# Performance work log

Hardware: AMD Instinct MI355X
Metric: run time of the kernel (lower is better)

## Reference

```python
import jax, jax.numpy as jnp
import numpy as np

N_HEADS = 4
SIGMA = 6.0
T_IN = 12
T_TOTAL = 24


def setup_inputs() -> dict:
    key = jax.random.key(0)
    k1, k2, k3, k4, k5 = jax.random.split(key, 5)
    B, T, N, C, K = 16, T_IN, 5000, 4, 16
    x = jax.random.normal(k1, (B, T, N, C), dtype=jnp.float32)
    dists = jax.random.uniform(k2, (N, K), dtype=jnp.float32) * 10.0  # kNN distances
    neighbors = jax.random.randint(k3, (N, K), 0, N)                  # kNN indices
    d_in = T * N_HEADS                   # 48
    d_out = T_TOTAL - T_IN               # 12
    W = jax.random.normal(k4, (d_in, d_out), dtype=jnp.float32) * (1.0 / np.sqrt(d_in))
    b = jax.random.normal(k5, (d_out,), dtype=jnp.float32) * 0.01
    return {"x": x, "dists": dists, "W": W, "b": b, "neighbors": neighbors}


def reference(x, dists, W, b, neighbors):
    B, T, N, C = x.shape
    H = N_HEADS
    # lambda_h = h/H for h = 1..H
    lam = jnp.arange(1, H + 1, dtype=x.dtype) / H                     # [H]
    # weights[n,k,h] = exp(-d_{nk}^2 * lam_h / sigma^2)
    w = jnp.exp(-(dists ** 2)[:, :, None] * lam / (SIGMA ** 2))       # [N,K,H]
    # gather neighbor features: [B,T,N,K,C]
    xg = x[:, :, neighbors, :]
    # distance-weighted aggregation over neighbors -> [B,T,N,H,C]
    agg = jnp.einsum('btnkc,nkh->btnhc', xg, w)
    # permute (0,2,4,1,3) -> [B,N,C,T,H], flatten last two -> [B,N,C,T*H]
    feat = jnp.transpose(agg, (0, 2, 4, 1, 3)).reshape(B, N, C, T * H)
    # shrink: Linear + ReLU -> [B,N,C,T_TOTAL-T]
    y = jax.nn.relu(feat @ W + b)
    # -> [B, T_TOTAL-T, N, C]
    y = jnp.transpose(y, (0, 3, 1, 2))
    return jnp.concatenate([x, y], axis=1)                            # [B,T_TOTAL,N,C]
```

## Files before the change

### kernel.cpp

```cpp
#include <hip/hip_runtime.h>

#define Bz 16
#define Tin 12
#define Ttot 24
#define NN 5000
#define Cc 4
#define KK 16
#define HH 4
#define OO 12
#define TH 48
#define BT 192
#define G  8
#define JJ 24

typedef float nfloat4 __attribute__((ext_vector_type(4)));

__device__ __forceinline__ float4 nt_load4(const float4* p) {
    nfloat4 v = __builtin_nontemporal_load((const nfloat4*)p);
    return *(float4*)&v;
}
__device__ __forceinline__ void nt_store4(float4 v, float4* p) {
    __builtin_nontemporal_store(*(nfloat4*)&v, (nfloat4*)p);
}

#define K1_NB 64
#define K1_BT 24

__global__ __launch_bounds__(256) void transpose_concat_kernel(
    const float4* __restrict__ x4,
    float4* __restrict__ xT2,
    float4* __restrict__ out4)
{
    __shared__ float4 tile[K1_BT][K1_NB + 1];
    const int n0  = blockIdx.x * K1_NB;
    const int g   = blockIdx.y;
    const int bt0 = g * K1_BT;
    const int rem = min(K1_NB, NN - n0);
    const int tid = threadIdx.x;

    #pragma unroll
    for (int r = 0; r < (K1_NB * K1_BT) / 256; r++) {
        int tau = r * 256 + tid;
        int j = tau / K1_NB;
        int i = tau % K1_NB;
        if (i < rem) {
            int bt = bt0 + j;
            float4 v = nt_load4(&x4[(size_t)bt * NN + n0 + i]);
            tile[j][i] = v;
            int b = bt / Tin, t = bt - b * Tin;
            nt_store4(v, &out4[(size_t)(b * Ttot + t) * NN + n0 + i]);
        }
    }
    __syncthreads();

    #pragma unroll
    for (int r = 0; r < (K1_NB * K1_BT) / 256; r++) {
        int tau = r * 256 + tid;
        int i = tau / K1_BT;
        int j = tau - i * K1_BT;
        if (i < rem) {
            xT2[((size_t)g * NN + (n0 + i)) * JJ + j] = tile[j][i];
        }
    }
}

#define NPB 8
#define FST 5
#define FSB 61
#define FSN 123

__global__ __launch_bounds__(192) void gnn_main_kernel(
    const float4* __restrict__ xT2,
    const float* __restrict__ dists,
    const float* __restrict__ W,
    const float* __restrict__ bias,
    const int*   __restrict__ nbrs,
    float4* __restrict__ out4)
{
    __shared__ float4 feat[NPB * FSN];
    __shared__ float4 w4_s[NPB][KK];
    __shared__ float  W_s[TH * OO];
    __shared__ float  bias_s[OO];
    __shared__ int    nbroff_s[NPB][KK];

    const int bid = blockIdx.x;
    const int g   = bid & 7;
    const int n0  = (bid >> 3) * NPB;
    const int tid = threadIdx.x;

    for (int i = tid; i < TH * OO; i += 192) W_s[i] = W[i];
    if (tid < OO) bias_s[tid] = bias[tid];
    if (tid < NPB * KK) {
        int nl = tid >> 4, k = tid & 15;
        nbroff_s[nl][k] = nbrs[(n0 + nl) * KK + k] * (JJ * (int)sizeof(float4));
        float d = dists[(n0 + nl) * KK + k];
        float p = expf(-(d * d) * (1.0f / 144.0f));
        float4 wv;
        wv.x = p;
        wv.y = p * p;
        wv.z = wv.y * p;
        wv.w = wv.y * wv.y;
        w4_s[nl][k] = wv;
    }
    __syncthreads();

    {
        const int nl  = tid / JJ;
        const int j   = tid - nl * JJ;
        const int b_l = j / Tin;
        const int t   = j - b_l * Tin;
        const char* xgb = (const char*)xT2 + (size_t)g * (NN * JJ * sizeof(float4));
        const unsigned j16 = (unsigned)j * (unsigned)sizeof(float4);

        float4 a0 = {0,0,0,0}, a1 = {0,0,0,0}, a2 = {0,0,0,0}, a3 = {0,0,0,0};
        #pragma unroll
        for (int k = 0; k < KK; k++) {
            unsigned off = (unsigned)nbroff_s[nl][k] + j16;
            float4 xv = *(const float4*)(xgb + off);
            float4 wv = w4_s[nl][k];
            a0.x += wv.x * xv.x; a0.y += wv.x * xv.y; a0.z += wv.x * xv.z; a0.w += wv.x * xv.w;
            a1.x += wv.y * xv.x; a1.y += wv.y * xv.y; a1.z += wv.y * xv.z; a1.w += wv.y * xv.w;
            a2.x += wv.z * xv.x; a2.y += wv.z * xv.y; a2.z += wv.z * xv.z; a2.w += wv.z * xv.w;
            a3.x += wv.w * xv.x; a3.y += wv.w * xv.y; a3.z += wv.w * xv.z; a3.w += wv.w * xv.w;
        }
        const int base = nl * FSN + b_l * FSB + t * FST;
        feat[base + 0] = a0;
        feat[base + 1] = a1;
        feat[base + 2] = a2;
        feat[base + 3] = a3;
    }
    __syncthreads();

    {
        const int nl  = tid & 7;
        const int bo  = tid >> 3;
        const int b_l = bo / OO;
        const int o   = bo - b_l * OO;
        const float bz = bias_s[o];
        float4 acc = {bz, bz, bz, bz};
        const int fbase = nl * FSN + b_l * FSB;
        #pragma unroll
        for (int t = 0; t < Tin; t++) {
            #pragma unroll
            for (int h = 0; h < HH; h++) {
                float  wv = W_s[(t * HH + h) * OO + o];
                float4 f  = feat[fbase + t * FST + h];
                acc.x += wv * f.x; acc.y += wv * f.y;
                acc.z += wv * f.z; acc.w += wv * f.w;
            }
        }
        acc.x = fmaxf(acc.x, 0.0f); acc.y = fmaxf(acc.y, 0.0f);
        acc.z = fmaxf(acc.z, 0.0f); acc.w = fmaxf(acc.w, 0.0f);
        const int b = g * 2 + b_l;
        nt_store4(acc, &out4[(size_t)(b * Ttot + Tin + o) * NN + n0 + nl]);
    }
}

extern "C" void kernel_launch(void* const* d_in, const int* in_sizes, int n_in,
                              void* d_out, int out_size, void* d_ws, size_t ws_size,
                              hipStream_t stream) {
    const float* x     = (const float*)d_in[0];
    const float* dists = (const float*)d_in[1];
    const float* W     = (const float*)d_in[2];
    const float* bias  = (const float*)d_in[3];
    const int*   nbrs  = (const int*)d_in[4];
    float4* out4 = (float4*)d_out;
    float4* xT2  = (float4*)d_ws;

    dim3 g1((NN + K1_NB - 1) / K1_NB, G);
    hipLaunchKernelGGL(transpose_concat_kernel, g1, dim3(256), 0, stream,
                       (const float4*)x, xT2, out4);

    hipLaunchKernelGGL(gnn_main_kernel, dim3((NN / NPB) * G), dim3(192), 0, stream,
                       (const float4*)xT2, dists, W, bias, nbrs, out4);
}
```

Before: 107.9 us.

## Re-layout gathered features per channel and fuse linear layer into registers

The workspace is now laid out per node as [c][b][t], so each thread gathers 12 contiguous time steps for one channel and batch. Per-head aggregates for all time steps stay in registers. The linear layer then runs straight from those registers against a transposed W in LDS, removing the shared-memory feat staging and the second barrier. Packed float2 math is used, blocks now cover 40 nodes with 320 threads, and output stores become scalar strided writes instead of float4 nontemporal stores.

Result: slower. 112.0 us (+3.8%).

```diff
diff --git a/kernel.cpp b/kernel.cpp
--- a/kernel.cpp
+++ b/kernel.cpp
@@ -1,19 +1,17 @@
 #include <hip/hip_runtime.h>
 
-#define Bz 16
 #define Tin 12
 #define Ttot 24
 #define NN 5000
-#define Cc 4
 #define KK 16
 #define HH 4
 #define OO 12
 #define TH 48
-#define BT 192
 #define G  8
 #define JJ 24
 
 typedef float nfloat4 __attribute__((ext_vector_type(4)));
+typedef float f2 __attribute__((ext_vector_type(2)));
 
 __device__ __forceinline__ float4 nt_load4(const float4* p) {
     nfloat4 v = __builtin_nontemporal_load((const nfloat4*)p);
@@ -28,7 +26,7 @@
 
 __global__ __launch_bounds__(256) void transpose_concat_kernel(
     const float4* __restrict__ x4,
-    float4* __restrict__ xT2,
+    float* __restrict__ xT3,
     float4* __restrict__ out4)
 {
     __shared__ float4 tile[K1_BT][K1_NB + 1];
@@ -53,106 +51,118 @@
     }
     __syncthreads();
 
+    float4* xT3g4 = (float4*)(xT3 + (size_t)g * NN * 96);
     #pragma unroll
-    for (int r = 0; r < (K1_NB * K1_BT) / 256; r++) {
-        int tau = r * 256 + tid;
-        int i = tau / K1_BT;
-        int j = tau - i * K1_BT;
+    for (int r = 0; r < 6; r++) {
+        int u = r * 256 + tid;
+        int i = u / 24;
+        int remu = u - i * 24;
         if (i < rem) {
-            xT2[((size_t)g * NN + (n0 + i)) * JJ + j] = tile[j][i];
+            int c  = remu / 6;
+            int s  = remu - c * 6;
+            int bl = s / 3;
+            int tq = s - bl * 3;
+            int j0 = bl * 12 + tq * 4;
+            float4 o;
+            o.x = ((const float*)&tile[j0 + 0][i])[c];
+            o.y = ((const float*)&tile[j0 + 1][i])[c];
+            o.z = ((const float*)&tile[j0 + 2][i])[c];
+            o.w = ((const float*)&tile[j0 + 3][i])[c];
+            xT3g4[(size_t)(n0 + i) * 24 + remu] = o;
         }
     }
 }
 
-#define NPB 8
-#define FST 5
-#define FSB 61
-#define FSN 123
+#define NPB 40
+#define NTH 320
 
-__global__ __launch_bounds__(192) void gnn_main_kernel(
-    const float4* __restrict__ xT2,
+__global__ __launch_bounds__(NTH) void gnn_main_kernel(
+    const float* __restrict__ xT3,
     const float* __restrict__ dists,
     const float* __restrict__ W,
     const float* __restrict__ bias,
     const int*   __restrict__ nbrs,
-    float4* __restrict__ out4)
+    float* __restrict__ outf)
 {
-    __shared__ float4 feat[NPB * FSN];
-    __shared__ float4 w4_s[NPB][KK];
-    __shared__ float  W_s[TH * OO];
+    __shared__ float4 w4_s[NPB][KK + 1];
+    __shared__ int    nbroff_s[NPB][KK + 1];
+    __shared__ __align__(16) float Wt_s[OO * TH];
     __shared__ float  bias_s[OO];
-    __shared__ int    nbroff_s[NPB][KK];
 
     const int bid = blockIdx.x;
     const int g   = bid & 7;
     const int n0  = (bid >> 3) * NPB;
     const int tid = threadIdx.x;
 
-    for (int i = tid; i < TH * OO; i += 192) W_s[i] = W[i];
+    for (int i = tid; i < OO * TH; i += NTH) {
+        int o = i / TH;
+        int r = i - o * TH;
+        int h = r / Tin;
+        int t = r - h * Tin;
+        Wt_s[i] = W[(t * HH + h) * OO + o];
+    }
     if (tid < OO) bias_s[tid] = bias[tid];
-    if (tid < NPB * KK) {
-        int nl = tid >> 4, k = tid & 15;
-        nbroff_s[nl][k] = nbrs[(n0 + nl) * KK + k] * (JJ * (int)sizeof(float4));
+    #pragma unroll
+    for (int r = 0; r < 2; r++) {
+        int u = r * NTH + tid;
+        int nl = u >> 4, k = u & 15;
+        nbroff_s[nl][k] = nbrs[(n0 + nl) * KK + k] * 384;
         float d = dists[(n0 + nl) * KK + k];
         float p = expf(-(d * d) * (1.0f / 144.0f));
         float4 wv;
-        wv.x = p;
-        wv.y = p * p;
-        wv.z = wv.y * p;
-        wv.w = wv.y * wv.y;
+        wv.x = p; wv.y = p * p; wv.z = wv.y * p; wv.w = wv.y * wv.y;
         w4_s[nl][k] = wv;
     }
     __syncthreads();
 
-    {
-        const int nl  = tid / JJ;
-        const int j   = tid - nl * JJ;
-        const int b_l = j / Tin;
-        const int t   = j - b_l * Tin;
-        const char* xgb = (const char*)xT2 + (size_t)g * (NN * JJ * sizeof(float4));
-        const unsigned j16 = (unsigned)j * (unsigned)sizeof(float4);
+    const int nl  = tid >> 3;
+    const int rr  = tid & 7;
+    const int c   = rr & 3;
+    const int b_l = rr >> 2;
+    const char* xgb = (const char*)xT3 + (size_t)g * (NN * 96 * 4);
+    const unsigned sl = (unsigned)(c * 2 + b_l) * 48u;
 
-        float4 a0 = {0,0,0,0}, a1 = {0,0,0,0}, a2 = {0,0,0,0}, a3 = {0,0,0,0};
+    f2 fp[HH][6];
+    #pragma unroll
+    for (int h = 0; h < HH; h++)
         #pragma unroll
-        for (int k = 0; k < KK; k++) {
-            unsigned off = (unsigned)nbroff_s[nl][k] + j16;
-            float4 xv = *(const float4*)(xgb + off);
-            float4 wv = w4_s[nl][k];
-            a0.x += wv.x * xv.x; a0.y += wv.x * xv.y; a0.z += wv.x * xv.z; a0.w += wv.x * xv.w;
-            a1.x += wv.y * xv.x; a1.y += wv.y * xv.y; a1.z += wv.y * xv.z; a1.w += wv.y * xv.w;
-            a2.x += wv.z * xv.x; a2.y += wv.z * xv.y; a2.z += wv.z * xv.z; a2.w += wv.z * xv.w;
-            a3.x += wv.w * xv.x; a3.y += wv.w * xv.y; a3.z += wv.w * xv.z; a3.w += wv.w * xv.w;
-        }
-        const int base = nl * FSN + b_l * FSB + t * FST;
-        feat[base + 0] = a0;
-        feat[base + 1] = a1;
-        feat[base + 2] = a2;
-        feat[base + 3] = a3;
+        for (int tp = 0; tp < 6; tp++) fp[h][tp] = f2{0.f, 0.f};
+
+    #pragma unroll
+    for (int k = 0; k < KK; k++) {
+        unsigned off = (unsigned)nbroff_s[nl][k] + sl;
+        const nfloat4* px = (const nfloat4*)(xgb + off);
+        nfloat4 x0 = px[0], x1 = px[1], x2 = px[2];
+        float4 wv = w4_s[nl][k];
+        f2 xp[6] = { f2{x0.x, x0.y}, f2{x0.z, x0.w},
+                     f2{x1.x, x1.y}, f2{x1.z, x1.w},
+                     f2{x2.x, x2.y}, f2{x2.z, x2.w} };
+        f2 wp[HH] = { f2{wv.x, wv.x}, f2{wv.y, wv.y},
+                      f2{wv.z, wv.z}, f2{wv.w, wv.w} };
+        #pragma unroll
+        for (int h = 0; h < HH; h++)
+            #pragma unroll
+            for (int tp = 0; tp < 6; tp++)
+                fp[h][tp] += wp[h] * xp[tp];
     }
-    __syncthreads();
 
-    {
-        const int nl  = tid & 7;
-        const int bo  = tid >> 3;
-        const int b_l = bo / OO;
-        const int o   = bo - b_l * OO;
-        const float bz = bias_s[o];
-        float4 acc = {bz, bz, bz, bz};
-        const int fbase = nl * FSN + b_l * FSB;
+    const int b = g * 2 + b_l;
+    const size_t outbase = ((size_t)(b * Ttot + Tin) * NN + (n0 + nl)) * 4 + c;
+    #pragma unroll
+    for (int o = 0; o < OO; o++) {
+        f2 acc = f2{0.f, 0.f};
         #pragma unroll
-        for (int t = 0; t < Tin; t++) {
+        for (int h = 0; h < HH; h++) {
             #pragma unroll
-            for (int h = 0; h < HH; h++) {
-                float  wv = W_s[(t * HH + h) * OO + o];
-                float4 f  = feat[fbase + t * FST + h];
-                acc.x += wv * f.x; acc.y += wv * f.y;
-                acc.z += wv * f.z; acc.w += wv * f.w;
+            for (int qq = 0; qq < 3; qq++) {
+                nfloat4 wq = *(const nfloat4*)&Wt_s[o * TH + h * Tin + qq * 4];
+                acc += f2{wq.x, wq.y} * fp[h][2 * qq];
+                acc += f2{wq.z, wq.w} * fp[h][2 * qq + 1];
             }
         }
-        acc.x = fmaxf(acc.x, 0.0f); acc.y = fmaxf(acc.y, 0.0f);
-        acc.z = fmaxf(acc.z, 0.0f); acc.w = fmaxf(acc.w, 0.0f);
-        const int b = g * 2 + b_l;
-        nt_store4(acc, &out4[(size_t)(b * Ttot + Tin + o) * NN + n0 + nl]);
+        float y = acc.x + acc.y + bias_s[o];
+        y = fmaxf(y, 0.f);
+        outf[outbase + (size_t)o * (NN * 4)] = y;
     }
 }
 
@@ -165,12 +175,12 @@
     const float* bias  = (const float*)d_in[3];
     const int*   nbrs  = (const int*)d_in[4];
     float4* out4 = (float4*)d_out;
-    float4* xT2  = (float4*)d_ws;
+    float*  xT3  = (float*)d_ws;
 
     dim3 g1((NN + K1_NB - 1) / K1_NB, G);
     hipLaunchKernelGGL(transpose_concat_kernel, g1, dim3(256), 0, stream,
-                       (const float4*)x, xT2, out4);
+                       (const float4*)x, xT3, out4);
 
-    hipLaunchKernelGGL(gnn_main_kernel, dim3((NN / NPB) * G), dim3(192), 0, stream,
-                       (const float4*)xT2, dists, W, bias, nbrs, out4);
+    hipLaunchKernelGGL(gnn_main_kernel, dim3((NN / NPB) * G), dim3(NTH), 0, stream,
+                       xT3, dists, W, bias, nbrs, (float*)d_out);
 }
```
